# Performance work log

Hardware: AMD Instinct MI355X
Metric: run time of the kernel (lower is better)

## Reference

```python
import jax, jax.numpy as jnp
import numpy as np

B, S, D, H, E, K = 8, 2048, 1024, 2048, 8, 2


def setup_inputs() -> dict:
    key = jax.random.key(0)
    k0, k1, k2, k3, k4 = jax.random.split(key, 5)
    x = jax.random.normal(k0, (B, S, D), jnp.float32)
    gate_w = jax.random.normal(k1, (E, D), jnp.float32) * (D ** -0.5)
    w1 = jax.random.normal(k2, (E, H, D), jnp.float32) * (D ** -0.5)
    w3 = jax.random.normal(k3, (E, H, D), jnp.float32) * (D ** -0.5)
    w2 = jax.random.normal(k4, (E, D, H), jnp.float32) * (H ** -0.5)
    return {"x": x, "gate_w": gate_w, "w1": w1, "w3": w3, "w2": w2, "k": K}


def reference(x, gate_w, w1, w3, w2, k):
    # Flatten tokens: [B, S, D] -> [T, D]
    x2 = x.reshape(-1, x.shape[-1])
    T = x2.shape[0]
    n_exp = gate_w.shape[0]
    # Gating: top-k logits, softmax over the k selected (in float32, cast back)
    logits = x2 @ gate_w.T                                  # [T, E]
    top_w, sel = jax.lax.top_k(logits, k)                   # [T, k] each
    top_w = jax.nn.softmax(top_w.astype(jnp.float32), axis=1).astype(x.dtype)
    # Dense combine weights [T, E]: zero for unselected experts (faithful to
    # the gather/scatter-add loop; topk indices are unique per token).
    cw = jnp.zeros((T, n_exp), x.dtype).at[jnp.arange(T)[:, None], sel].add(top_w)
    # Per-expert SwiGLU FFN, accumulated with combine weights.
    out = jnp.zeros_like(x2)
    for e in range(n_exp):  # fixed small structural loop over experts
        h = jax.nn.silu(x2 @ w1[e].T) * (x2 @ w3[e].T)      # [T, H]
        out = out + cw[:, e:e + 1] * (h @ w2[e].T)          # [T, D]
    return out.reshape(x.shape)
```

## Files before the change

kernel.cpp:

```cpp
#include <hip/hip_runtime.h>
#include <hip/hip_bf16.h>
#include <cstdint>


#define T_TOK 16384
#define DIM   1024
#define HID   2048
#define NEXP  8
#define MAX_TILES 264

typedef __bf16 bf16;
typedef bf16  bf16x8 __attribute__((ext_vector_type(8)));
typedef bf16  bf16x4 __attribute__((ext_vector_type(4)));
typedef float f32x16 __attribute__((ext_vector_type(16)));

__device__ __forceinline__ void async_cp16(const void* g, void* l) {
  __builtin_amdgcn_global_load_lds((const __attribute__((address_space(1))) void*)g,
                                   (__attribute__((address_space(3))) void*)l, 16, 0, 0);
}

__global__ __launch_bounds__(256) void zero_kernel(float4* __restrict__ out4, int n4,
                                                   int* __restrict__ ctrl) {
  const int i = blockIdx.x * 256 + threadIdx.x;
  if (i < n4) out4[i] = float4{0.f, 0.f, 0.f, 0.f};
  if (blockIdx.x == 0 && threadIdx.x < 64) ctrl[threadIdx.x] = 0;
}

__global__ __launch_bounds__(256) void cvt_kernel(const float* __restrict__ in,
                                                  bf16* __restrict__ out, int n4) {
  const int i = blockIdx.x * 256 + threadIdx.x;
  if (i < n4) {
    const float4 v = ((const float4*)in)[i];
    bf16x4 o;
    o[0] = (bf16)v.x; o[1] = (bf16)v.y; o[2] = (bf16)v.z; o[3] = (bf16)v.w;
    ((bf16x4*)out)[i] = o;
  }
}

__global__ __launch_bounds__(64) void gate_kernel(const float* __restrict__ x,
                                                  const float* __restrict__ gw,
                                                  int* __restrict__ sel,
                                                  float* __restrict__ selw) {
  const int t = blockIdx.x;
  const int lane = threadIdx.x;
  const float* xr = x + (size_t)t * DIM;
  float acc[NEXP];
#pragma unroll
  for (int e = 0; e < NEXP; e++) acc[e] = 0.f;
  for (int i = lane; i < DIM; i += 64) {
    const float xv = xr[i];
#pragma unroll
    for (int e = 0; e < NEXP; e++) acc[e] += xv * gw[e * DIM + i];
  }
#pragma unroll
  for (int e = 0; e < NEXP; e++) {
#pragma unroll
    for (int m = 1; m < 64; m <<= 1) acc[e] += __shfl_xor(acc[e], m);
  }
  if (lane == 0) {
    int e0 = 0; float l0 = acc[0];
#pragma unroll
    for (int e = 1; e < NEXP; e++) if (acc[e] > l0) { l0 = acc[e]; e0 = e; }
    int e1 = -1; float l1 = -3.4e38f;
#pragma unroll
    for (int e = 0; e < NEXP; e++) if (e != e0 && acc[e] > l1) { l1 = acc[e]; e1 = e; }
    const float ex = expf(l1 - l0);
    const float w0 = 1.f / (1.f + ex);
    sel[t * 2] = e0;  sel[t * 2 + 1] = e1;
    selw[t * 2] = w0; selw[t * 2 + 1] = 1.f - w0;
  }
}

__global__ __launch_bounds__(256) void count_kernel(const int* __restrict__ sel,
                                                    int* __restrict__ counts) {
  const int i = blockIdx.x * 256 + threadIdx.x;
  const int lane = threadIdx.x & 63;
  const int e = sel[i];
#pragma unroll
  for (int ee = 0; ee < NEXP; ee++) {
    const unsigned long long mask = __ballot(e == ee);
    if (e == ee) {
      const int leader = __ffsll(mask) - 1;
      if (lane == leader) atomicAdd(&counts[ee], __popcll(mask));
    }
  }
}

__global__ void tilemap_kernel(const int* __restrict__ counts, int* __restrict__ segoff,
                               int* __restrict__ tile_e, int* __restrict__ tile_m,
                               int* __restrict__ ntiles) {
  if (threadIdx.x == 0 && blockIdx.x == 0) {
    int off = 0, nt = 0;
    for (int e = 0; e < NEXP; e++) {
      segoff[e] = off;
      const int c = counts[e];
      for (int m = 0; m < c; m += 128) { tile_e[nt] = e; tile_m[nt] = m; nt++; }
      off += c;
    }
    segoff[NEXP] = off;
    ntiles[0] = nt;
  }
}

__global__ __launch_bounds__(256) void fill_kernel(const int* __restrict__ sel,
                                                   const float* __restrict__ selw,
                                                   const int* __restrict__ segoff,
                                                   int* __restrict__ fill,
                                                   int* __restrict__ tokl,
                                                   float* __restrict__ wl) {
  const int t = blockIdx.x * 256 + threadIdx.x;
  const int lane = threadIdx.x & 63;
#pragma unroll
  for (int s = 0; s < 2; s++) {
    const int e = sel[t * 2 + s];
    const float w = selw[t * 2 + s];
    for (int ee = 0; ee < NEXP; ee++) {
      const unsigned long long mask = __ballot(e == ee);
      if (e == ee) {
        const int leader = __ffsll(mask) - 1;
        const int cnt = __popcll(mask);
        int base = 0;
        if (lane == leader) base = atomicAdd(&fill[ee], cnt);
        base = __shfl(base, leader);
        const int pos = base + __popcll(mask & ((1ull << lane) - 1ull));
        const int idx = segoff[ee] + pos;
        tokl[idx] = t;
        wl[idx] = w;
      }
    }
  }
}

__global__ __launch_bounds__(256) void gemm_act_kernel(
    const bf16* __restrict__ xb, const bf16* __restrict__ w1b, const bf16* __restrict__ w3b,
    const int* __restrict__ tokl, const int* __restrict__ counts, const int* __restrict__ segoff,
    const int* __restrict__ tile_e, const int* __restrict__ tile_m, const int* __restrict__ ntiles,
    bf16* __restrict__ act) {
  const int tile = blockIdx.y;
  if (tile >= *ntiles) return;
  const int e   = tile_e[tile];
  const int m0  = tile_m[tile];
  const int n0  = blockIdx.x * 64;
  const int Ne  = counts[e];
  const int seg = segoff[e];

  __shared__ bf16 As[128 * 64];
  __shared__ bf16 Bs1[64 * 64];
  __shared__ bf16 Bs3[64 * 64];

  const int tid = threadIdx.x;
  const int lane = tid & 63;
  const int wv = tid >> 6;
  const int sr = tid >> 3;
  const int scb = (tid & 7) ^ (sr & 7);

  const bf16* aptr[4];
#pragma unroll
  for (int i = 0; i < 4; i++) {
    int m = m0 + sr + 32 * i; if (m > Ne - 1) m = Ne - 1;
    aptr[i] = xb + (size_t)tokl[seg + m] * DIM + scb * 8;
  }
  const bf16 *b1p[2], *b3p[2];
#pragma unroll
  for (int i = 0; i < 2; i++) {
    const int n = n0 + sr + 32 * i;
    b1p[i] = w1b + ((size_t)e * HID + n) * DIM + scb * 8;
    b3p[i] = w3b + ((size_t)e * HID + n) * DIM + scb * 8;
  }

  f32x16 acc1[2], acc3[2];
#pragma unroll
  for (int i = 0; i < 2; i++)
#pragma unroll
    for (int j = 0; j < 16; j++) { acc1[i][j] = 0.f; acc3[i][j] = 0.f; }

  const int lwm = (wv & 1) * 64;
  const int lwn = (wv >> 1) * 32;
  const int l31 = lane & 31;
  const int lhi = lane >> 5;
  const int l7  = l31 & 7;

  for (int k0 = 0; k0 < DIM; k0 += 64) {
#pragma unroll
    for (int i = 0; i < 4; i++)
      async_cp16(aptr[i] + k0, (char*)As + i * 4096 + tid * 16);
#pragma unroll
    for (int i = 0; i < 2; i++) {
      async_cp16(b1p[i] + k0, (char*)Bs1 + i * 4096 + tid * 16);
      async_cp16(b3p[i] + k0, (char*)Bs3 + i * 4096 + tid * 16);
    }
    __syncthreads();
#pragma unroll
    for (int ks = 0; ks < 4; ks++) {
      const int swz = (((ks * 2 + lhi) ^ l7) * 8);
      bf16x8 a0 = *(const bf16x8*)(As + (lwm + l31) * 64 + swz);
      bf16x8 a1 = *(const bf16x8*)(As + (lwm + 32 + l31) * 64 + swz);
      bf16x8 b1 = *(const bf16x8*)(Bs1 + (lwn + l31) * 64 + swz);
      bf16x8 b3 = *(const bf16x8*)(Bs3 + (lwn + l31) * 64 + swz);
      acc1[0] = __builtin_amdgcn_mfma_f32_32x32x16_bf16(a0, b1, acc1[0], 0, 0, 0);
      acc3[0] = __builtin_amdgcn_mfma_f32_32x32x16_bf16(a0, b3, acc3[0], 0, 0, 0);
      acc1[1] = __builtin_amdgcn_mfma_f32_32x32x16_bf16(a1, b1, acc1[1], 0, 0, 0);
      acc3[1] = __builtin_amdgcn_mfma_f32_32x32x16_bf16(a1, b3, acc3[1], 0, 0, 0);
    }
    __syncthreads();
  }

#pragma unroll
  for (int ms = 0; ms < 2; ms++) {
#pragma unroll
    for (int r = 0; r < 16; r++) {
      const int row = lwm + 32 * ms + (r & 3) + 8 * (r >> 2) + 4 * lhi;
      const int m = m0 + row;
      if (m < Ne) {
        const float h1 = acc1[ms][r];
        const float h3 = acc3[ms][r];
        const float sv = h1 / (1.f + __expf(-h1)) * h3;
        act[(size_t)(seg + m) * HID + (n0 + lwn + l31)] = (bf16)sv;
      }
    }
  }
}

__global__ __launch_bounds__(256) void gemm_out_kernel(
    const bf16* __restrict__ act, const bf16* __restrict__ w2b,
    const int* __restrict__ tokl, const float* __restrict__ wl,
    const int* __restrict__ counts, const int* __restrict__ segoff,
    const int* __restrict__ tile_e, const int* __restrict__ tile_m, const int* __restrict__ ntiles,
    float* __restrict__ out) {
  const int tile = blockIdx.y;
  if (tile >= *ntiles) return;
  const int e   = tile_e[tile];
  const int m0  = tile_m[tile];
  const int n0  = blockIdx.x * 128;
  const int Ne  = counts[e];
  const int seg = segoff[e];

  __shared__ bf16 As[128 * 64];
  __shared__ bf16 Bs[128 * 64];
  __shared__ int   sh_tok[128];
  __shared__ float sh_w[128];

  const int tid = threadIdx.x;
  const int lane = tid & 63;
  const int wv = tid >> 6;
  const int sr = tid >> 3;
  const int scb = (tid & 7) ^ (sr & 7);

  if (tid < 128) {
    const int m = m0 + tid;
    if (m < Ne) { sh_tok[tid] = tokl[seg + m]; sh_w[tid] = wl[seg + m]; }
    else        { sh_tok[tid] = -1;            sh_w[tid] = 0.f; }
  }

  const bf16* aptr[4];
#pragma unroll
  for (int i = 0; i < 4; i++) {
    int m = m0 + sr + 32 * i; if (m > Ne - 1) m = Ne - 1;
    aptr[i] = act + (size_t)(seg + m) * HID + scb * 8;
  }
  const bf16* bptr[4];
#pragma unroll
  for (int i = 0; i < 4; i++) {
    const int d = n0 + sr + 32 * i;
    bptr[i] = w2b + ((size_t)e * DIM + d) * HID + scb * 8;
  }

  f32x16 acc[4];
#pragma unroll
  for (int i = 0; i < 4; i++)
#pragma unroll
    for (int j = 0; j < 16; j++) acc[i][j] = 0.f;

  const int lwm = (wv & 1) * 64;
  const int lwn = (wv >> 1) * 64;
  const int l31 = lane & 31;
  const int lhi = lane >> 5;
  const int l7  = l31 & 7;

  for (int k0 = 0; k0 < HID; k0 += 64) {
#pragma unroll
    for (int i = 0; i < 4; i++)
      async_cp16(aptr[i] + k0, (char*)As + i * 4096 + tid * 16);
#pragma unroll
    for (int i = 0; i < 4; i++)
      async_cp16(bptr[i] + k0, (char*)Bs + i * 4096 + tid * 16);
    __syncthreads();
#pragma unroll
    for (int ks = 0; ks < 4; ks++) {
      const int swz = (((ks * 2 + lhi) ^ l7) * 8);
      bf16x8 a0 = *(const bf16x8*)(As + (lwm + l31) * 64 + swz);
      bf16x8 a1 = *(const bf16x8*)(As + (lwm + 32 + l31) * 64 + swz);
      bf16x8 b0 = *(const bf16x8*)(Bs + (lwn + l31) * 64 + swz);
      bf16x8 b1 = *(const bf16x8*)(Bs + (lwn + 32 + l31) * 64 + swz);
      acc[0] = __builtin_amdgcn_mfma_f32_32x32x16_bf16(a0, b0, acc[0], 0, 0, 0);
      acc[1] = __builtin_amdgcn_mfma_f32_32x32x16_bf16(a0, b1, acc[1], 0, 0, 0);
      acc[2] = __builtin_amdgcn_mfma_f32_32x32x16_bf16(a1, b0, acc[2], 0, 0, 0);
      acc[3] = __builtin_amdgcn_mfma_f32_32x32x16_bf16(a1, b1, acc[3], 0, 0, 0);
    }
    __syncthreads();
  }

#pragma unroll
  for (int mi = 0; mi < 2; mi++) {
#pragma unroll
    for (int ni = 0; ni < 2; ni++) {
#pragma unroll
      for (int r = 0; r < 16; r++) {
        const int row = lwm + 32 * mi + (r & 3) + 8 * (r >> 2) + 4 * lhi;
        const int tok = sh_tok[row];
        if (tok >= 0) {
          const int col = n0 + lwn + 32 * ni + l31;
          atomicAdd(&out[(size_t)tok * DIM + col], sh_w[row] * acc[mi * 2 + ni][r]);
        }
      }
    }
  }
}

extern "C" void kernel_launch(void* const* d_in, const int* in_sizes, int n_in,
                              void* d_out, int out_size, void* d_ws, size_t ws_size,
                              hipStream_t stream) {
  const float* x  = (const float*)d_in[0];
  const float* gw = (const float*)d_in[1];
  const float* w1 = (const float*)d_in[2];
  const float* w3 = (const float*)d_in[3];
  const float* w2 = (const float*)d_in[4];
  float* out = (float*)d_out;

  char* ws = (char*)d_ws;
  size_t off = 0;
  auto alloc = [&](size_t bytes) -> char* {
    char* p = ws + off; off += (bytes + 255) & ~(size_t)255; return p;
  };

  int* ctrl = (int*)alloc(4096);
  int* counts = ctrl;
  int* fill   = ctrl + 8;
  int* segoff = ctrl + 16;
  int* ntiles = ctrl + 32;
  int* tile_e = ctrl + 64;
  int* tile_m = ctrl + 512;
  int*   sel  = (int*)alloc((size_t)T_TOK * 2 * 4);
  float* selw = (float*)alloc((size_t)T_TOK * 2 * 4);
  int*   tokl = (int*)alloc((size_t)2 * T_TOK * 4);
  float* wl   = (float*)alloc((size_t)2 * T_TOK * 4);

  bf16* act  = (bf16*)alloc((size_t)2 * T_TOK * HID * 2);
  bf16* w1b  = (bf16*)alloc((size_t)NEXP * HID * DIM * 2);
  bf16* w3b  = (bf16*)alloc((size_t)NEXP * HID * DIM * 2);
  bf16* xb   = (bf16*)alloc((size_t)T_TOK * DIM * 2);
  bf16* w2b  = xb;
  (void)ws_size; (void)in_sizes; (void)n_in; (void)out_size;

  zero_kernel<<<T_TOK * DIM / 4 / 256, 256, 0, stream>>>((float4*)out, T_TOK * DIM / 4, ctrl);

  cvt_kernel<<<16384, 256, 0, stream>>>(x,  xb,  T_TOK * DIM / 4);
  cvt_kernel<<<16384, 256, 0, stream>>>(w1, w1b, NEXP * HID * DIM / 4);
  cvt_kernel<<<16384, 256, 0, stream>>>(w3, w3b, NEXP * HID * DIM / 4);

  gate_kernel<<<T_TOK, 64, 0, stream>>>(x, gw, sel, selw);
  count_kernel<<<2 * T_TOK / 256, 256, 0, stream>>>(sel, counts);
  tilemap_kernel<<<1, 64, 0, stream>>>(counts, segoff, tile_e, tile_m, ntiles);
  fill_kernel<<<T_TOK / 256, 256, 0, stream>>>(sel, selw, segoff, fill, tokl, wl);

  gemm_act_kernel<<<dim3(HID / 64, MAX_TILES), 256, 0, stream>>>(
      xb, w1b, w3b, tokl, counts, segoff, tile_e, tile_m, ntiles, act);

  cvt_kernel<<<16384, 256, 0, stream>>>(w2, w2b, NEXP * DIM * HID / 4);

  gemm_out_kernel<<<dim3(DIM / 128, MAX_TILES), 256, 0, stream>>>(
      act, w2b, tokl, wl, counts, segoff, tile_e, tile_m, ntiles, out);
}
```

Before: 1.010 ms.

## Enlarge gate/up GEMM tiles to 256x128 with double-buffered LDS pipelining

```diff
diff --git a/kernel.cpp b/kernel.cpp
--- a/kernel.cpp
+++ b/kernel.cpp
@@ -8,6 +8,7 @@
 #define HID   2048
 #define NEXP  8
 #define MAX_TILES 264
+#define MAX_T256  136
 
 typedef __bf16 bf16;
 typedef bf16  bf16x8 __attribute__((ext_vector_type(8)));
@@ -88,17 +89,21 @@
 
 __global__ void tilemap_kernel(const int* __restrict__ counts, int* __restrict__ segoff,
                                int* __restrict__ tile_e, int* __restrict__ tile_m,
-                               int* __restrict__ ntiles) {
+                               int* __restrict__ ntiles,
+                               int* __restrict__ tile_e2, int* __restrict__ tile_m2,
+                               int* __restrict__ ntiles2) {
   if (threadIdx.x == 0 && blockIdx.x == 0) {
-    int off = 0, nt = 0;
+    int off = 0, nt = 0, nt2 = 0;
     for (int e = 0; e < NEXP; e++) {
       segoff[e] = off;
       const int c = counts[e];
       for (int m = 0; m < c; m += 128) { tile_e[nt] = e; tile_m[nt] = m; nt++; }
+      for (int m = 0; m < c; m += 256) { tile_e2[nt2] = e; tile_m2[nt2] = m; nt2++; }
       off += c;
     }
     segoff[NEXP] = off;
     ntiles[0] = nt;
+    ntiles2[0] = nt2;
   }
 }
 
@@ -131,91 +136,106 @@
   }
 }
 
-__global__ __launch_bounds__(256) void gemm_act_kernel(
+__global__ __launch_bounds__(512, 2) void gemm_act_kernel(
     const bf16* __restrict__ xb, const bf16* __restrict__ w1b, const bf16* __restrict__ w3b,
     const int* __restrict__ tokl, const int* __restrict__ counts, const int* __restrict__ segoff,
-    const int* __restrict__ tile_e, const int* __restrict__ tile_m, const int* __restrict__ ntiles,
+    const int* __restrict__ tile_e2, const int* __restrict__ tile_m2, const int* __restrict__ ntiles2,
     bf16* __restrict__ act) {
   const int tile = blockIdx.y;
-  if (tile >= *ntiles) return;
-  const int e   = tile_e[tile];
-  const int m0  = tile_m[tile];
-  const int n0  = blockIdx.x * 64;
+  if (tile >= *ntiles2) return;
+  const int e   = tile_e2[tile];
+  const int m0  = tile_m2[tile];
+  const int n0  = blockIdx.x * 128;
   const int Ne  = counts[e];
   const int seg = segoff[e];
 
-  __shared__ bf16 As[128 * 64];
-  __shared__ bf16 Bs1[64 * 64];
-  __shared__ bf16 Bs3[64 * 64];
-
-  const int tid = threadIdx.x;
+  extern __shared__ char smem[];
+
+  const int tid  = threadIdx.x;
   const int lane = tid & 63;
-  const int wv = tid >> 6;
-  const int sr = tid >> 3;
-  const int scb = (tid & 7) ^ (sr & 7);
+  const int wv   = tid >> 6;
+  const int sr   = tid >> 3;
+  const int scb  = (tid & 7) ^ (sr & 7);
 
   const bf16* aptr[4];
 #pragma unroll
   for (int i = 0; i < 4; i++) {
-    int m = m0 + sr + 32 * i; if (m > Ne - 1) m = Ne - 1;
+    int m = m0 + sr + 64 * i; if (m > Ne - 1) m = Ne - 1;
     aptr[i] = xb + (size_t)tokl[seg + m] * DIM + scb * 8;
   }
-  const bf16 *b1p[2], *b3p[2];
-#pragma unroll
-  for (int i = 0; i < 2; i++) {
-    const int n = n0 + sr + 32 * i;
-    b1p[i] = w1b + ((size_t)e * HID + n) * DIM + scb * 8;
-    b3p[i] = w3b + ((size_t)e * HID + n) * DIM + scb * 8;
-  }
-
-  f32x16 acc1[2], acc3[2];
-#pragma unroll
-  for (int i = 0; i < 2; i++)
-#pragma unroll
-    for (int j = 0; j < 16; j++) { acc1[i][j] = 0.f; acc3[i][j] = 0.f; }
-
-  const int lwm = (wv & 1) * 64;
-  const int lwn = (wv >> 1) * 32;
+  const bf16* bptr[4];
+#pragma unroll
+  for (int i = 0; i < 4; i++) {
+    const bf16* wsel = ((sr >> 5) & 1) ? w3b : w1b;
+    bptr[i] = wsel + ((size_t)e * HID + n0 + 32 * i + (sr & 31)) * DIM + scb * 8;
+  }
+
+  f32x16 acc[4][2];
+#pragma unroll
+  for (int i = 0; i < 4; i++)
+#pragma unroll
+    for (int j = 0; j < 2; j++)
+#pragma unroll
+      for (int r = 0; r < 16; r++) acc[i][j][r] = 0.f;
+
+  const int wmBase = (wv >> 2) * 128;
+  const int wnBase = (wv & 3) * 64;
   const int l31 = lane & 31;
   const int lhi = lane >> 5;
   const int l7  = l31 & 7;
 
-  for (int k0 = 0; k0 < DIM; k0 += 64) {
-#pragma unroll
-    for (int i = 0; i < 4; i++)
-      async_cp16(aptr[i] + k0, (char*)As + i * 4096 + tid * 16);
-#pragma unroll
-    for (int i = 0; i < 2; i++) {
-      async_cp16(b1p[i] + k0, (char*)Bs1 + i * 4096 + tid * 16);
-      async_cp16(b3p[i] + k0, (char*)Bs3 + i * 4096 + tid * 16);
-    }
-    __syncthreads();
-#pragma unroll
-    for (int ks = 0; ks < 4; ks++) {
+#pragma unroll
+  for (int i = 0; i < 4; i++) {
+    async_cp16(aptr[i],          smem +         i * 8192 + tid * 16);
+    async_cp16(bptr[i],          smem + 32768 + i * 8192 + tid * 16);
+  }
+
+  for (int t = 0; t < DIM / 64; ++t) {
+    const bf16* Acur = (const bf16*)(smem + (t & 1) * 65536);
+    const bf16* Bcur = Acur + 16384;
+    char* Anx = smem + ((t + 1) & 1) * 65536;
+    char* Bnx = Anx + 32768;
+    const int kn = (t < DIM / 64 - 1 ? t + 1 : t) * 64;
+#pragma unroll
+    for (int ks = 0; ks < 4; ++ks) {
+      async_cp16(aptr[ks] + kn, Anx + ks * 8192 + tid * 16);
+      async_cp16(bptr[ks] + kn, Bnx + ks * 8192 + tid * 16);
+      if (ks == 0) {
+        asm volatile("s_waitcnt vmcnt(2)\n\ts_barrier" ::: "memory");
+      }
       const int swz = (((ks * 2 + lhi) ^ l7) * 8);
-      bf16x8 a0 = *(const bf16x8*)(As + (lwm + l31) * 64 + swz);
-      bf16x8 a1 = *(const bf16x8*)(As + (lwm + 32 + l31) * 64 + swz);
-      bf16x8 b1 = *(const bf16x8*)(Bs1 + (lwn + l31) * 64 + swz);
-      bf16x8 b3 = *(const bf16x8*)(Bs3 + (lwn + l31) * 64 + swz);
-      acc1[0] = __builtin_amdgcn_mfma_f32_32x32x16_bf16(a0, b1, acc1[0], 0, 0, 0);
-      acc3[0] = __builtin_amdgcn_mfma_f32_32x32x16_bf16(a0, b3, acc3[0], 0, 0, 0);
-      acc1[1] = __builtin_amdgcn_mfma_f32_32x32x16_bf16(a1, b1, acc1[1], 0, 0, 0);
-      acc3[1] = __builtin_amdgcn_mfma_f32_32x32x16_bf16(a1, b3, acc3[1], 0, 0, 0);
-    }
-    __syncthreads();
-  }
-
-#pragma unroll
-  for (int ms = 0; ms < 2; ms++) {
+      bf16x8 a0 = *(const bf16x8*)(Acur + (wmBase +  0 + l31) * 64 + swz);
+      bf16x8 a1 = *(const bf16x8*)(Acur + (wmBase + 32 + l31) * 64 + swz);
+      bf16x8 a2 = *(const bf16x8*)(Acur + (wmBase + 64 + l31) * 64 + swz);
+      bf16x8 a3 = *(const bf16x8*)(Acur + (wmBase + 96 + l31) * 64 + swz);
+      bf16x8 b0 = *(const bf16x8*)(Bcur + (wnBase +  0 + l31) * 64 + swz);
+      bf16x8 b1 = *(const bf16x8*)(Bcur + (wnBase + 32 + l31) * 64 + swz);
+      __builtin_amdgcn_s_setprio(1);
+      acc[0][0] = __builtin_amdgcn_mfma_f32_32x32x16_bf16(a0, b0, acc[0][0], 0, 0, 0);
+      acc[0][1] = __builtin_amdgcn_mfma_f32_32x32x16_bf16(a0, b1, acc[0][1], 0, 0, 0);
+      acc[1][0] = __builtin_amdgcn_mfma_f32_32x32x16_bf16(a1, b0, acc[1][0], 0, 0, 0);
+      acc[1][1] = __builtin_amdgcn_mfma_f32_32x32x16_bf16(a1, b1, acc[1][1], 0, 0, 0);
+      acc[2][0] = __builtin_amdgcn_mfma_f32_32x32x16_bf16(a2, b0, acc[2][0], 0, 0, 0);
+      acc[2][1] = __builtin_amdgcn_mfma_f32_32x32x16_bf16(a2, b1, acc[2][1], 0, 0, 0);
+      acc[3][0] = __builtin_amdgcn_mfma_f32_32x32x16_bf16(a3, b0, acc[3][0], 0, 0, 0);
+      acc[3][1] = __builtin_amdgcn_mfma_f32_32x32x16_bf16(a3, b1, acc[3][1], 0, 0, 0);
+      __builtin_amdgcn_s_setprio(0);
+      asm volatile("s_barrier" ::: "memory");
+    }
+  }
+
+  const int col = n0 + (wv & 3) * 32 + l31;
+#pragma unroll
+  for (int mi = 0; mi < 4; mi++) {
 #pragma unroll
     for (int r = 0; r < 16; r++) {
-      const int row = lwm + 32 * ms + (r & 3) + 8 * (r >> 2) + 4 * lhi;
+      const int row = wmBase + 32 * mi + (r & 3) + 8 * (r >> 2) + 4 * lhi;
       const int m = m0 + row;
       if (m < Ne) {
-        const float h1 = acc1[ms][r];
-        const float h3 = acc3[ms][r];
+        const float h1 = acc[mi][0][r];
+        const float h3 = acc[mi][1][r];
         const float sv = h1 / (1.f + __expf(-h1)) * h3;
-        act[(size_t)(seg + m) * HID + (n0 + lwn + l31)] = (bf16)sv;
+        act[(size_t)(seg + m) * HID + col] = (bf16)sv;
       }
     }
   }
@@ -333,13 +353,16 @@
     char* p = ws + off; off += (bytes + 255) & ~(size_t)255; return p;
   };
 
-  int* ctrl = (int*)alloc(4096);
-  int* counts = ctrl;
-  int* fill   = ctrl + 8;
-  int* segoff = ctrl + 16;
-  int* ntiles = ctrl + 32;
-  int* tile_e = ctrl + 64;
-  int* tile_m = ctrl + 512;
+  int* ctrl = (int*)alloc(8192);
+  int* counts  = ctrl;
+  int* fill    = ctrl + 8;
+  int* segoff  = ctrl + 16;
+  int* ntiles  = ctrl + 32;
+  int* ntiles2 = ctrl + 33;
+  int* tile_e  = ctrl + 64;
+  int* tile_m  = ctrl + 512;
+  int* tile_e2 = ctrl + 1024;
+  int* tile_m2 = ctrl + 1536;
   int*   sel  = (int*)alloc((size_t)T_TOK * 2 * 4);
   float* selw = (float*)alloc((size_t)T_TOK * 2 * 4);
   int*   tokl = (int*)alloc((size_t)2 * T_TOK * 4);
@@ -352,6 +375,9 @@
   bf16* w2b  = xb;
   (void)ws_size; (void)in_sizes; (void)n_in; (void)out_size;
 
+  hipFuncSetAttribute((const void*)gemm_act_kernel,
+                      hipFuncAttributeMaxDynamicSharedMemorySize, 131072);
+
   zero_kernel<<<T_TOK * DIM / 4 / 256, 256, 0, stream>>>((float4*)out, T_TOK * DIM / 4, ctrl);
 
   cvt_kernel<<<16384, 256, 0, stream>>>(x,  xb,  T_TOK * DIM / 4);
@@ -360,11 +386,12 @@
 
   gate_kernel<<<T_TOK, 64, 0, stream>>>(x, gw, sel, selw);
   count_kernel<<<2 * T_TOK / 256, 256, 0, stream>>>(sel, counts);
-  tilemap_kernel<<<1, 64, 0, stream>>>(counts, segoff, tile_e, tile_m, ntiles);
+  tilemap_kernel<<<1, 64, 0, stream>>>(counts, segoff, tile_e, tile_m, ntiles,
+                                       tile_e2, tile_m2, ntiles2);
   fill_kernel<<<T_TOK / 256, 256, 0, stream>>>(sel, selw, segoff, fill, tokl, wl);
 
-  gemm_act_kernel<<<dim3(HID / 64, MAX_TILES), 256, 0, stream>>>(
-      xb, w1b, w3b, tokl, counts, segoff, tile_e, tile_m, ntiles, act);
+  gemm_act_kernel<<<dim3(HID / 128, MAX_T256), 512, 131072, stream>>>(
+      xb, w1b, w3b, tokl, counts, segoff, tile_e2, tile_m2, ntiles2, act);
 
   cvt_kernel<<<16384, 256, 0, stream>>>(w2, w2b, NEXP * DIM * HID / 4);
 
```

Measured after the change: 982.2 us. 2.7% less time.
